# Kernel optimization log

Hardware: AMD Instinct MI355X
Metric: run time of the kernel (lower is better)

The kernel has to match this reference:

```python
import jax, jax.numpy as jnp
import numpy as np

B, N, E = 2, 2048, 1024
H = 16
D = E // H  # head_dim = 64
MLP = 4096
EPS = 1e-5


def _layernorm(x, g, b):
    mu = jnp.mean(x, axis=-1, keepdims=True)
    var = jnp.var(x, axis=-1, keepdims=True)
    return (x - mu) * jax.lax.rsqrt(var + EPS) * g + b


def setup_inputs() -> dict:
    key = jax.random.key(0)
    ks = jax.random.split(key, 12)
    s_e = 1.0 / np.sqrt(E)
    s_m = 1.0 / np.sqrt(MLP)
    return {
        "x": jax.random.normal(ks[0], (B, N, E), jnp.float32),
        "w_qkv": jax.random.uniform(ks[1], (E, 3 * E), jnp.float32, -s_e, s_e),
        "b_qkv": jax.random.uniform(ks[2], (3 * E,), jnp.float32, -s_e, s_e),
        "w_proj": jax.random.uniform(ks[3], (E, E), jnp.float32, -s_e, s_e),
        "b_proj": jax.random.uniform(ks[4], (E,), jnp.float32, -s_e, s_e),
        "g1": jnp.ones((E,), jnp.float32),
        "beta1": jnp.zeros((E,), jnp.float32),
        "g2": jnp.ones((E,), jnp.float32),
        "beta2": jnp.zeros((E,), jnp.float32),
        "w_fc1": jax.random.uniform(ks[5], (E, MLP), jnp.float32, -s_e, s_e),
        "b_fc1": jax.random.uniform(ks[6], (MLP,), jnp.float32, -s_e, s_e),
        "w_fc2": jax.random.uniform(ks[7], (MLP, E), jnp.float32, -s_m, s_m),
        "b_fc2": jax.random.uniform(ks[8], (E,), jnp.float32, -s_m, s_m),
    }


def reference(x, w_qkv, b_qkv, w_proj, b_proj, g1, beta1, g2, beta2,
              w_fc1, b_fc1, w_fc2, b_fc2):
    scale = D ** (-0.5)
    # --- attention block (pre-norm) ---
    h = _layernorm(x, g1, beta1)
    qkv = (h @ w_qkv + b_qkv).reshape(B, N, 3, H, D)
    q, k, v = (qkv[:, :, i].transpose(0, 2, 1, 3) for i in range(3))  # [B,H,N,D]
    scores = jnp.einsum("bhnd,bhmd->bhnm", q, k) * scale  # [B,H,N,N]
    attn = jax.nn.softmax(scores, axis=-1)
    out = jnp.einsum("bhnm,bhmd->bhnd", attn, v)
    out = out.transpose(0, 2, 1, 3).reshape(B, N, E)
    x = x + (out @ w_proj + b_proj)
    # --- MLP block (pre-norm, exact GELU as in torch default) ---
    h = _layernorm(x, g2, beta2)
    h = jax.nn.gelu(h @ w_fc1 + b_fc1, approximate=False) @ w_fc2 + b_fc2
    return x + h
```

## Files before the change

kernel.cpp:

```cpp
#include <hip/hip_runtime.h>
#include <hip/hip_bf16.h>
#include <cmath>


typedef __hip_bfloat16 bf16;
typedef __bf16 bf16x8 __attribute__((ext_vector_type(8)));
typedef __bf16 bf16x4v __attribute__((ext_vector_type(4)));
typedef float  f32x4  __attribute__((ext_vector_type(4)));

#define CB 2
#define CN 2048
#define CE 1024
#define CH 16
#define CD 64
#define CMLP 4096
#define CM (CB*CN)

#define PS 136

#define QPRE 0.18033688011112042f
#if __has_builtin(__builtin_amdgcn_exp2f)
#define EXP2(s) __builtin_amdgcn_exp2f(s)
#else
#define EXP2(s) __expf((s)*0.69314718055994531f)
#endif

__device__ __forceinline__ float b2f(bf16 v){ return __bfloat162float(v); }
__device__ __forceinline__ bf16  f2b(float v){ return __float2bfloat16(v); }

__device__ __forceinline__ void gl_lds16(const void* g, void* l){
  __builtin_amdgcn_global_load_lds((__attribute__((address_space(1))) void*)g,
                                   (__attribute__((address_space(3))) void*)l,
                                   16, 0, 0);
}

#define FENCE asm volatile("" ::: "memory")
#define BAR   do{ FENCE; __builtin_amdgcn_s_barrier(); FENCE; }while(0)
#define VMW6  asm volatile("s_waitcnt vmcnt(6)" ::: "memory")
#define VMW0  asm volatile("s_waitcnt vmcnt(0)" ::: "memory")

__global__ __launch_bounds__(256) void transpose4_k(
  const float* __restrict__ i0, bf16* __restrict__ o0,
  const float* __restrict__ i1, bf16* __restrict__ o1,
  const float* __restrict__ i2, bf16* __restrict__ o2,
  const float* __restrict__ i3, bf16* __restrict__ o3)
{
  __shared__ float tile[32][33];
  int t = blockIdx.x;
  const float* in; bf16* out; int K, N, nx;
  if(t < 3072){            in=i0; out=o0; K=1024; N=3072; nx=96; }
  else if(t < 4096){ t-=3072; in=i1; out=o1; K=1024; N=1024; nx=32; }
  else if(t < 8192){ t-=4096; in=i2; out=o2; K=1024; N=4096; nx=128; }
  else {             t-=8192; in=i3; out=o3; K=4096; N=1024; nx=32; }
  const int n0 = (t%nx)*32, k0 = (t/nx)*32;
  const int tx = threadIdx.x & 31;
  const int ty = threadIdx.x >> 5;
  #pragma unroll
  for(int i=0;i<32;i+=8) tile[ty+i][tx] = in[(size_t)(k0+ty+i)*N + n0+tx];
  __syncthreads();
  #pragma unroll
  for(int i=0;i<32;i+=8) out[(size_t)(n0+ty+i)*K + k0+tx] = f2b(tile[tx][ty+i]);
}

__global__ __launch_bounds__(256) void ln_k(const float* __restrict__ x,
                                            const float* __restrict__ g,
                                            const float* __restrict__ be,
                                            bf16* __restrict__ out){
  const int row = blockIdx.x;
  const int t = threadIdx.x;
  const float4 v4 = ((const float4*)(x + (size_t)row*CE))[t];
  float v[4] = {v4.x, v4.y, v4.z, v4.w};
  float s=0.f, s2=0.f;
  #pragma unroll
  for(int i=0;i<4;i++){ s+=v[i]; s2+=v[i]*v[i]; }
  #pragma unroll
  for(int off=32; off>0; off>>=1){ s += __shfl_down(s,off); s2 += __shfl_down(s2,off); }
  __shared__ float red[8];
  __shared__ float mu_s, rs_s;
  const int wv=t>>6, ln=t&63;
  if(ln==0){ red[wv]=s; red[4+wv]=s2; }
  __syncthreads();
  if(t==0){
    float S=red[0]+red[1]+red[2]+red[3], S2=red[4]+red[5]+red[6]+red[7];
    float mu=S/CE;
    mu_s=mu; rs_s=rsqrtf(S2/CE - mu*mu + 1e-5f);
  }
  __syncthreads();
  const float mu=mu_s, rs=rs_s;
  #pragma unroll
  for(int i=0;i<4;i++){
    int c=t*4+i;
    out[(size_t)row*CE+c] = f2b((v[i]-mu)*rs*g[c] + be[c]);
  }
}

#define EP_QKV 0
#define EP_RES 1
#define EP_GELU 2

template<int MODE, int BN>
__global__ __launch_bounds__(256,2) void gemm_k(
  const bf16* __restrict__ A, const bf16* __restrict__ BT,
  const float* __restrict__ bias, const float* __restrict__ res,
  float* __restrict__ Cf, bf16* __restrict__ Cb,
  bf16* __restrict__ Cq, bf16* __restrict__ Ck, bf16* __restrict__ Cv,
  int Ksz, int Nsz)
{
  constexpr int NJ = BN/32;
  constexpr int NBUF = (BN==64) ? 3 : 2;
  __shared__ __align__(16) bf16 Alds[NBUF][128*64];
  __shared__ __align__(16) bf16 Blds[NBUF][BN*64];
  const int tid = threadIdx.x;
  const int wave = tid>>6, lane = tid&63;
  const int m16 = lane&15, quad = lane>>4;
  const int wi = wave>>1, wj = wave&1;

  const int lin = blockIdx.x + gridDim.x*blockIdx.y;
  const int m_idx = (lin&7) + 8*((lin>>3)&3);
  const int n_idx = lin>>5;
  const size_t m0 = (size_t)m_idx*128;
  const size_t n0 = (size_t)n_idx*BN;

  f32x4 acc[4][NJ] = {};

  const int srow8 = lane>>3;
  const int schk  = ((lane&7)^srow8)*8;
  const bf16* pA = A  + (m0 + 32*wave      + srow8)*(size_t)Ksz + schk;
  const bf16* pB = BT + (n0 + (BN/4)*wave  + srow8)*(size_t)Ksz + schk;

  auto stage = [&](int buf, const bf16* gA, const bf16* gB){
    bf16* lA = &Alds[buf][wave*2048];
    bf16* lB = &Blds[buf][wave*(BN*16)];
    #pragma unroll
    for(int j=0;j<4;j++)  gl_lds16(gA + (size_t)(j*8)*Ksz, lA + j*512);
    #pragma unroll
    for(int j=0;j<NJ;j++) gl_lds16(gB + (size_t)(j*8)*Ksz, lB + j*512);
  };
  auto compute = [&](int buf){
    #pragma unroll
    for(int w=0;w<2;w++){
      const int sw = (m16&7);
      bf16x8 af[4], bfr[NJ];
      #pragma unroll
      for(int i=0;i<4;i++){
        const int row = wi*64+16*i+m16;
        af[i] = *(const bf16x8*)(&Alds[buf][row*64 + ((w*4+quad)^sw)*8]);
      }
      #pragma unroll
      for(int j=0;j<NJ;j++){
        const int row = wj*(BN/2)+16*j+m16;
        bfr[j] = *(const bf16x8*)(&Blds[buf][row*64 + ((w*4+quad)^sw)*8]);
      }
      #pragma unroll
      for(int i=0;i<4;i++)
        #pragma unroll
        for(int j=0;j<NJ;j++)
          acc[i][j] = __builtin_amdgcn_mfma_f32_16x16x32_bf16(af[i], bfr[j], acc[i][j], 0,0,0);
    }
  };

  const int kIters = Ksz/64;
  if constexpr (BN==64){
    stage(0, pA, pB); pA += 64; pB += 64;
    stage(1, pA, pB); pA += 64; pB += 64;
    int bc = 0, bs = 2;
    for(int kb=0; kb<kIters; ++kb){
      if(kb==kIters-1){ VMW0; } else { VMW6; }
      BAR;
      if(kb+2<kIters){ stage(bs, pA, pB); pA += 64; pB += 64; }
      compute(bc);
      bc = (bc==2)?0:bc+1;
      bs = (bs==2)?0:bs+1;
    }
  } else {
    stage(0, pA, pB); pA += 64; pB += 64;
    for(int kb=0; kb<kIters; ++kb){
      __syncthreads();
      if(kb+1<kIters){ stage((kb+1)&1, pA, pB); pA += 64; pB += 64; }
      compute(kb&1);
    }
  }

  #pragma unroll
  for(int i=0;i<4;i++){
    #pragma unroll
    for(int j=0;j<NJ;j++){
      const int col = (int)n0 + wj*(BN/2) + 16*j + m16;
      const float bcol = bias[col];
      #pragma unroll
      for(int r=0;r<4;r++){
        const int row = (int)m0 + wi*64 + 16*i + quad*4 + r;
        float v = acc[i][j][r] + bcol;
        if constexpr (MODE==EP_QKV){
          const int b = row>>11, n = row&2047;
          const int which = col>>10, cc = col&1023;
          const int h = cc>>6, d = cc&63;
          if(which==0)      Cq[(((size_t)(b*CH+h))*CN+n)*CD + d] = f2b(v*QPRE);
          else if(which==1) Ck[(((size_t)(b*CH+h))*CN+n)*CD + d] = f2b(v);
          else              Cv[(((size_t)(b*CH+h))*CD+d)*CN + n] = f2b(v);
        } else if constexpr (MODE==EP_RES){
          v += res[(size_t)row*Nsz+col];
          Cf[(size_t)row*Nsz+col] = v;
        } else {
          const float u2 = 1.5957691216f*(v + 0.044715f*v*v*v);
          v = v * (1.f/(1.f + __expf(-u2)));
          Cb[(size_t)row*Nsz+col] = f2b(v);
        }
      }
    }
  }
}

__global__ __launch_bounds__(256,2) void attn_k(
  const bf16* __restrict__ Q, const bf16* __restrict__ Kx,
  const bf16* __restrict__ Vt, bf16* __restrict__ O)
{
  const int lin = blockIdx.x + gridDim.x*blockIdx.y;
  const int bh = (lin&7) + 8*(lin>>7);
  const int qblk = (lin>>3)&15;
  const int b = bh>>4, h = bh&15;
  const int tid = threadIdx.x;
  const int wave = tid>>6, lane = tid&63;
  const int m16 = lane&15, quad = lane>>4;
  const int sw = m16&7;
  const int q0 = qblk*128 + wave*32;

  const bf16* Qb = Q  + (size_t)bh*CN*CD;
  const bf16* Kb = Kx + (size_t)bh*CN*CD;
  const bf16* Vb = Vt + (size_t)bh*CD*CN;

  bf16x8 qf[2][2];
  #pragma unroll
  for(int g=0;g<2;g++){
    const bf16* qp = Qb + (size_t)(q0+g*16+m16)*CD + quad*8;
    qf[g][0] = *(const bf16x8*)(qp);
    qf[g][1] = *(const bf16x8*)(qp + 32);
  }

  bf16x8 onesv;
  #pragma unroll
  for(int i=0;i<8;i++) onesv[i] = (__bf16)1.0f;

  f32x4 lacc[2] = {};
  f32x4 oacc[2][4] = {};

  __shared__ __align__(16) bf16 Klds[128*64];
  __shared__ __align__(16) bf16 Vlds[64*128];
  __shared__ __align__(16) bf16 Plds[4][32*PS];
  bf16* Pw = &Plds[wave][0];

  const int krow = wave*32 + (lane>>3);
  const int kchk = (lane&7) ^ (lane>>3);
  const bf16* pK = Kb + (size_t)krow*CD + kchk*8;
  const int vrow = wave*16 + (lane>>4);
  const bf16* pV[4];
  #pragma unroll
  for(int j=0;j<4;j++){
    const int ck = (lane&15) ^ ((j*4 + (lane>>4)) & 7);
    pV[j] = Vb + (size_t)(vrow + j*4)*CN + ck*8;
  }
  bf16* lK = Klds + wave*2048;
  bf16* lV = Vlds + wave*2048;

  for(int kt=0; kt<CN; kt+=128){
    __syncthreads();
    #pragma unroll
    for(int j=0;j<4;j++){
      gl_lds16(pK + (size_t)j*8*CD, lK + j*512);
      gl_lds16(pV[j],               lV + j*512);
      pV[j] += 128;
    }
    pK += (size_t)128*CD;
    __syncthreads();

    f32x4 sf0[8], sf1[8];
    #pragma unroll
    for(int f=0;f<8;f++){
      const bf16* kb = Klds + (f*16+m16)*64;
      bf16x8 k0 = *(const bf16x8*)(kb + ((quad   ^ sw)*8));
      bf16x8 k1 = *(const bf16x8*)(kb + (((quad+4)^ sw)*8));
      f32x4 t0 = {}, t1 = {};
      t0 = __builtin_amdgcn_mfma_f32_16x16x32_bf16(k0, qf[0][0], t0, 0,0,0);
      t0 = __builtin_amdgcn_mfma_f32_16x16x32_bf16(k1, qf[0][1], t0, 0,0,0);
      t1 = __builtin_amdgcn_mfma_f32_16x16x32_bf16(k0, qf[1][0], t1, 0,0,0);
      t1 = __builtin_amdgcn_mfma_f32_16x16x32_bf16(k1, qf[1][1], t1, 0,0,0);
      sf0[f]=t0; sf1[f]=t1;
    }
    #pragma unroll
    for(int f=0;f<8;f++){
      bf16x4v p0, p1;
      #pragma unroll
      for(int r=0;r<4;r++){
        p0[r] = (__bf16)EXP2(sf0[f][r]);
        p1[r] = (__bf16)EXP2(sf1[f][r]);
      }
      *(bf16x4v*)(Pw + (size_t)m16*PS       + f*16 + quad*4) = p0;
      *(bf16x4v*)(Pw + (size_t)(16+m16)*PS  + f*16 + quad*4) = p1;
    }
    asm volatile("s_waitcnt lgkmcnt(0)" ::: "memory");
    #pragma unroll
    for(int c=0;c<4;c++){
      const bf16x8 ap0 = *(const bf16x8*)(Pw + (size_t)m16*PS      + c*32 + quad*8);
      const bf16x8 ap1 = *(const bf16x8*)(Pw + (size_t)(16+m16)*PS + c*32 + quad*8);
      lacc[0] = __builtin_amdgcn_mfma_f32_16x16x32_bf16(ap0, onesv, lacc[0], 0,0,0);
      lacc[1] = __builtin_amdgcn_mfma_f32_16x16x32_bf16(ap1, onesv, lacc[1], 0,0,0);
      #pragma unroll
      for(int dt=0;dt<4;dt++){
        const int d = dt*16+m16;
        bf16x8 bv = *(const bf16x8*)(Vlds + d*128 + (((c*4+quad) ^ sw)*8));
        oacc[0][dt] = __builtin_amdgcn_mfma_f32_16x16x32_bf16(ap0, bv, oacc[0][dt], 0,0,0);
        oacc[1][dt] = __builtin_amdgcn_mfma_f32_16x16x32_bf16(ap1, bv, oacc[1][dt], 0,0,0);
      }
    }
  }
  #pragma unroll
  for(int g=0;g<2;g++){
    float linv[4];
    #pragma unroll
    for(int r=0;r<4;r++) linv[r] = 1.f / lacc[g][r];
    #pragma unroll
    for(int dt=0;dt<4;dt++){
      #pragma unroll
      for(int r=0;r<4;r++){
        const int row = q0 + g*16 + quad*4 + r;
        O[((size_t)(b*CN+row))*CE + h*CD + dt*16 + m16] = f2b(oacc[g][dt][r]*linv[r]);
      }
    }
  }
}

extern "C" void kernel_launch(void* const* d_in, const int* in_sizes, int n_in,
                              void* d_out, int out_size, void* d_ws, size_t ws_size,
                              hipStream_t stream)
{
  (void)in_sizes; (void)n_in; (void)out_size; (void)ws_size;
  const float* x     = (const float*)d_in[0];
  const float* w_qkv = (const float*)d_in[1];
  const float* b_qkv = (const float*)d_in[2];
  const float* w_proj= (const float*)d_in[3];
  const float* b_proj= (const float*)d_in[4];
  const float* g1    = (const float*)d_in[5];
  const float* be1   = (const float*)d_in[6];
  const float* g2    = (const float*)d_in[7];
  const float* be2   = (const float*)d_in[8];
  const float* w_fc1 = (const float*)d_in[9];
  const float* b_fc1 = (const float*)d_in[10];
  const float* w_fc2 = (const float*)d_in[11];
  const float* b_fc2 = (const float*)d_in[12];
  float* out = (float*)d_out;

  char* ws = (char*)d_ws;
  size_t off = 0;
  auto alloc = [&](size_t bytes)->char*{
    char* p = ws + off;
    off += (bytes + 255) & ~(size_t)255;
    return p;
  };
  bf16* wqkvT = (bf16*)alloc((size_t)3072*1024*2);
  bf16* wprojT= (bf16*)alloc((size_t)1024*1024*2);
  bf16* wfc1T = (bf16*)alloc((size_t)4096*1024*2);
  bf16* wfc2T = (bf16*)alloc((size_t)1024*4096*2);
  bf16* h1    = (bf16*)alloc((size_t)CM*CE*2);
  bf16* q     = (bf16*)alloc((size_t)CM*CE*2);
  bf16* kk    = (bf16*)alloc((size_t)CM*CE*2);
  bf16* vT    = (bf16*)alloc((size_t)CM*CE*2);
  bf16* aO    = (bf16*)alloc((size_t)CM*CE*2);
  float* x2   = (float*)alloc((size_t)CM*CE*4);
  bf16* hmlp  = q;

  transpose4_k<<<12288,256,0,stream>>>(w_qkv, wqkvT, w_proj, wprojT,
                                       w_fc1, wfc1T, w_fc2, wfc2T);

  ln_k<<<CM,256,0,stream>>>(x, g1, be1, h1);
  gemm_k<EP_QKV,128><<<dim3(3072/128, CM/128),256,0,stream>>>(
      h1, wqkvT, b_qkv, nullptr, nullptr, nullptr, q, kk, vT, 1024, 3072);
  attn_k<<<dim3(CN/128, CB*CH),256,0,stream>>>(q, kk, vT, aO);
  gemm_k<EP_RES,64><<<dim3(1024/64, CM/128),256,0,stream>>>(
      aO, wprojT, b_proj, x, x2, nullptr, nullptr,nullptr,nullptr, 1024, 1024);
  ln_k<<<CM,256,0,stream>>>(x2, g2, be2, h1);
  gemm_k<EP_GELU,128><<<dim3(4096/128, CM/128),256,0,stream>>>(
      h1, wfc1T, b_fc1, nullptr, nullptr, hmlp, nullptr,nullptr,nullptr, 1024, 4096);
  gemm_k<EP_RES,64><<<dim3(1024/64, CM/128),256,0,stream>>>(
      hmlp, wfc2T, b_fc2, x2, out, nullptr, nullptr,nullptr,nullptr, 4096, 1024);
}
```

Before: 336.5 us.

## Add 128x128 triple-buffered GEMM kernel for projection and FC2 residual GEMMs

Adds a new GEMM kernel with 128x128 output tiles and a 64-wide K step, staged through three LDS buffers via direct global-to-LDS loads so two stages stay in flight. It replaces the 128x64-tile gemm_k for the attention-output projection and the FC2 residual GEMMs. The goal is more data reuse per block and deeper load/compute overlap. The cost is that the N=1024 GEMMs launch half as many blocks (256), which may leave compute units underused, and the large LDS footprint allows only one block per CU.

```diff
diff --git a/kernel.cpp b/kernel.cpp
--- a/kernel.cpp
+++ b/kernel.cpp
@@ -36,6 +36,7 @@
 
 #define FENCE asm volatile("" ::: "memory")
 #define BAR   do{ FENCE; __builtin_amdgcn_s_barrier(); FENCE; }while(0)
+#define VMW8  asm volatile("s_waitcnt vmcnt(8)" ::: "memory")
 #define VMW6  asm volatile("s_waitcnt vmcnt(6)" ::: "memory")
 #define VMW0  asm volatile("s_waitcnt vmcnt(0)" ::: "memory")
 
@@ -206,6 +207,87 @@
           v = v * (1.f/(1.f + __expf(-u2)));
           Cb[(size_t)row*Nsz+col] = f2b(v);
         }
+      }
+    }
+  }
+}
+
+__global__ __launch_bounds__(256,1) void gemmbig_k(
+  const bf16* __restrict__ A, const bf16* __restrict__ BT,
+  const float* __restrict__ bias, const float* __restrict__ res,
+  float* __restrict__ Cf, int Ksz, int Nsz)
+{
+  __shared__ __align__(16) bf16 Alds[3][128*64];
+  __shared__ __align__(16) bf16 Blds[3][128*64];
+  const int tid = threadIdx.x;
+  const int wave = tid>>6, lane = tid&63;
+  const int m16 = lane&15, quad = lane>>4;
+  const int sw = m16&7;
+  const int wi = wave>>1, wj = wave&1;
+
+  const int lin = blockIdx.x + gridDim.x*blockIdx.y;
+  const int m_idx = (lin&7) + 8*((lin>>3)&3);
+  const int n_idx = lin>>5;
+  const size_t m0 = (size_t)m_idx*128;
+  const size_t n0 = (size_t)n_idx*128;
+
+  f32x4 acc[4][4] = {};
+
+  const int srow8 = lane>>3;
+  const int schk  = ((lane&7)^srow8)*8;
+  const bf16* pA = A  + (m0 + 32*wave + srow8)*(size_t)Ksz + schk;
+  const bf16* pB = BT + (n0 + 32*wave + srow8)*(size_t)Ksz + schk;
+
+  auto stage = [&](int buf){
+    bf16* lA = &Alds[buf][wave*2048];
+    bf16* lB = &Blds[buf][wave*2048];
+    #pragma unroll
+    for(int j=0;j<4;j++){
+      gl_lds16(pA + (size_t)(j*8)*Ksz, lA + j*512);
+      gl_lds16(pB + (size_t)(j*8)*Ksz, lB + j*512);
+    }
+    pA += 64; pB += 64;
+  };
+  auto compute = [&](int buf){
+    #pragma unroll
+    for(int w=0;w<2;w++){
+      bf16x8 af[4], bfr[4];
+      #pragma unroll
+      for(int i=0;i<4;i++)
+        af[i] = *(const bf16x8*)(&Alds[buf][(wi*64+16*i+m16)*64 + ((w*4+quad)^sw)*8]);
+      #pragma unroll
+      for(int j=0;j<4;j++)
+        bfr[j] = *(const bf16x8*)(&Blds[buf][(wj*64+16*j+m16)*64 + ((w*4+quad)^sw)*8]);
+      #pragma unroll
+      for(int i=0;i<4;i++)
+        #pragma unroll
+        for(int j=0;j<4;j++)
+          acc[i][j] = __builtin_amdgcn_mfma_f32_16x16x32_bf16(af[i], bfr[j], acc[i][j], 0,0,0);
+    }
+  };
+
+  const int kIters = Ksz/64;
+  stage(0); stage(1);
+  int bc = 0, bs = 2;
+  for(int kb=0; kb<kIters; ++kb){
+    if(kb==kIters-1){ VMW0; } else { VMW8; }
+    BAR;
+    if(kb+2<kIters){ stage(bs); }
+    compute(bc);
+    bc = (bc==2)?0:bc+1;
+    bs = (bs==2)?0:bs+1;
+  }
+
+  #pragma unroll
+  for(int i=0;i<4;i++){
+    #pragma unroll
+    for(int j=0;j<4;j++){
+      const int col = (int)n0 + wj*64 + 16*j + m16;
+      const float bcol = bias[col];
+      #pragma unroll
+      for(int r=0;r<4;r++){
+        const int row = (int)m0 + wi*64 + 16*i + quad*4 + r;
+        Cf[(size_t)row*Nsz+col] = acc[i][j][r] + bcol + res[(size_t)row*Nsz+col];
       }
     }
   }
@@ -375,11 +457,11 @@
   gemm_k<EP_QKV,128><<<dim3(3072/128, CM/128),256,0,stream>>>(
       h1, wqkvT, b_qkv, nullptr, nullptr, nullptr, q, kk, vT, 1024, 3072);
   attn_k<<<dim3(CN/128, CB*CH),256,0,stream>>>(q, kk, vT, aO);
-  gemm_k<EP_RES,64><<<dim3(1024/64, CM/128),256,0,stream>>>(
-      aO, wprojT, b_proj, x, x2, nullptr, nullptr,nullptr,nullptr, 1024, 1024);
+  gemmbig_k<<<dim3(1024/128, CM/128),256,0,stream>>>(
+      aO, wprojT, b_proj, x, x2, 1024, 1024);
   ln_k<<<CM,256,0,stream>>>(x2, g2, be2, h1);
   gemm_k<EP_GELU,128><<<dim3(4096/128, CM/128),256,0,stream>>>(
       h1, wfc1T, b_fc1, nullptr, nullptr, hmlp, nullptr,nullptr,nullptr, 1024, 4096);
-  gemm_k<EP_RES,64><<<dim3(1024/64, CM/128),256,0,stream>>>(
-      hmlp, wfc2T, b_fc2, x2, out, nullptr, nullptr,nullptr,nullptr, 4096, 1024);
-}
+  gemmbig_k<<<dim3(1024/128, CM/128),256,0,stream>>>(
+      hmlp, wfc2T, b_fc2, x2, out, 4096, 1024);
+}
```

New measurement: 350.8 us. 1.04x slower.

## Double-buffer attention K/V tiles and fuse first layernorm into weight prep

Applied to the files above, without the earlier changes.

The attention kernel now uses 64-key tiles with two LDS buffers and prefetches the next K/V tile while computing on the current one. This drops one of the two barriers per iteration and overlaps global loads with MFMA work. Separately, the first layernorm is folded into the weight transpose launch as extra blocks, which removes one kernel launch. The smaller tiles double the number of loop iterations and barriers, and the double buffering relies on a single barrier being enough to protect buffer reuse.

```diff
diff --git a/kernel.cpp b/kernel.cpp
--- a/kernel.cpp
+++ b/kernel.cpp
@@ -16,7 +16,7 @@
 #define CMLP 4096
 #define CM (CB*CN)
 
-#define PS 136
+#define PS2 72
 
 #define QPRE 0.18033688011112042f
 #if __has_builtin(__builtin_amdgcn_exp2f)
@@ -39,22 +39,53 @@
 #define VMW6  asm volatile("s_waitcnt vmcnt(6)" ::: "memory")
 #define VMW0  asm volatile("s_waitcnt vmcnt(0)" ::: "memory")
 
-__global__ __launch_bounds__(256) void transpose4_k(
+__global__ __launch_bounds__(256) void prep_k(
   const float* __restrict__ i0, bf16* __restrict__ o0,
   const float* __restrict__ i1, bf16* __restrict__ o1,
   const float* __restrict__ i2, bf16* __restrict__ o2,
-  const float* __restrict__ i3, bf16* __restrict__ o3)
+  const float* __restrict__ i3, bf16* __restrict__ o3,
+  const float* __restrict__ x,  const float* __restrict__ g,
+  const float* __restrict__ be, bf16* __restrict__ lnout)
 {
   __shared__ float tile[32][33];
+  __shared__ float red[8];
+  __shared__ float mu_s, rs_s;
   int t = blockIdx.x;
+  const int tid = threadIdx.x;
+  if(t >= 12288){
+    const int row = t - 12288;
+    const float4 v4 = ((const float4*)(x + (size_t)row*CE))[tid];
+    float v[4] = {v4.x, v4.y, v4.z, v4.w};
+    float s=0.f, s2=0.f;
+    #pragma unroll
+    for(int i=0;i<4;i++){ s+=v[i]; s2+=v[i]*v[i]; }
+    #pragma unroll
+    for(int off=32; off>0; off>>=1){ s += __shfl_down(s,off); s2 += __shfl_down(s2,off); }
+    const int wv=tid>>6, ln=tid&63;
+    if(ln==0){ red[wv]=s; red[4+wv]=s2; }
+    __syncthreads();
+    if(tid==0){
+      float S=red[0]+red[1]+red[2]+red[3], S2=red[4]+red[5]+red[6]+red[7];
+      float mu=S/CE;
+      mu_s=mu; rs_s=rsqrtf(S2/CE - mu*mu + 1e-5f);
+    }
+    __syncthreads();
+    const float mu=mu_s, rs=rs_s;
+    #pragma unroll
+    for(int i=0;i<4;i++){
+      int c=tid*4+i;
+      lnout[(size_t)row*CE+c] = f2b((v[i]-mu)*rs*g[c] + be[c]);
+    }
+    return;
+  }
   const float* in; bf16* out; int K, N, nx;
   if(t < 3072){            in=i0; out=o0; K=1024; N=3072; nx=96; }
   else if(t < 4096){ t-=3072; in=i1; out=o1; K=1024; N=1024; nx=32; }
   else if(t < 8192){ t-=4096; in=i2; out=o2; K=1024; N=4096; nx=128; }
   else {             t-=8192; in=i3; out=o3; K=4096; N=1024; nx=32; }
   const int n0 = (t%nx)*32, k0 = (t/nx)*32;
-  const int tx = threadIdx.x & 31;
-  const int ty = threadIdx.x >> 5;
+  const int tx = tid & 31;
+  const int ty = tid >> 5;
   #pragma unroll
   for(int i=0;i<32;i+=8) tile[ty+i][tx] = in[(size_t)(k0+ty+i)*N + n0+tx];
   __syncthreads();
@@ -244,39 +275,37 @@
   f32x4 lacc[2] = {};
   f32x4 oacc[2][4] = {};
 
-  __shared__ __align__(16) bf16 Klds[128*64];
-  __shared__ __align__(16) bf16 Vlds[64*128];
-  __shared__ __align__(16) bf16 Plds[4][32*PS];
+  __shared__ __align__(16) bf16 Klds[2][64*64];
+  __shared__ __align__(16) bf16 Vlds[2][64*64];
+  __shared__ __align__(16) bf16 Plds[4][32*PS2];
   bf16* Pw = &Plds[wave][0];
 
-  const int krow = wave*32 + (lane>>3);
-  const int kchk = (lane&7) ^ (lane>>3);
-  const bf16* pK = Kb + (size_t)krow*CD + kchk*8;
-  const int vrow = wave*16 + (lane>>4);
-  const bf16* pV[4];
-  #pragma unroll
-  for(int j=0;j<4;j++){
-    const int ck = (lane&15) ^ ((j*4 + (lane>>4)) & 7);
-    pV[j] = Vb + (size_t)(vrow + j*4)*CN + ck*8;
-  }
-  bf16* lK = Klds + wave*2048;
-  bf16* lV = Vlds + wave*2048;
-
-  for(int kt=0; kt<CN; kt+=128){
+  const int srow8 = lane>>3;
+  const int kchk  = (lane&7) ^ srow8;
+  const bf16* pK = Kb + (size_t)(wave*16 + srow8)*CD + kchk*8;
+  const bf16* pV = Vb + (size_t)(wave*16 + srow8)*CN + kchk*8;
+  const int ldso = wave*1024;
+
+  auto stage = [&](int buf, int kt){
+    #pragma unroll
+    for(int j=0;j<2;j++){
+      gl_lds16(pK + ((size_t)kt + (size_t)j*8)*CD, &Klds[buf][ldso + j*512]);
+      gl_lds16(pV + (size_t)j*8*CN + kt,           &Vlds[buf][ldso + j*512]);
+    }
+  };
+
+  stage(0, 0);
+  const int nT = CN/64;
+  for(int t=0; t<nT; ++t){
     __syncthreads();
-    #pragma unroll
-    for(int j=0;j<4;j++){
-      gl_lds16(pK + (size_t)j*8*CD, lK + j*512);
-      gl_lds16(pV[j],               lV + j*512);
-      pV[j] += 128;
-    }
-    pK += (size_t)128*CD;
-    __syncthreads();
-
-    f32x4 sf0[8], sf1[8];
-    #pragma unroll
-    for(int f=0;f<8;f++){
-      const bf16* kb = Klds + (f*16+m16)*64;
+    if(t+1<nT) stage((t+1)&1, (t+1)*64);
+    const bf16* Kl = &Klds[t&1][0];
+    const bf16* Vl = &Vlds[t&1][0];
+
+    f32x4 sf0[4], sf1[4];
+    #pragma unroll
+    for(int f=0;f<4;f++){
+      const bf16* kb = Kl + (f*16+m16)*64;
       bf16x8 k0 = *(const bf16x8*)(kb + ((quad   ^ sw)*8));
       bf16x8 k1 = *(const bf16x8*)(kb + (((quad+4)^ sw)*8));
       f32x4 t0 = {}, t1 = {};
@@ -287,27 +316,27 @@
       sf0[f]=t0; sf1[f]=t1;
     }
     #pragma unroll
-    for(int f=0;f<8;f++){
+    for(int f=0;f<4;f++){
       bf16x4v p0, p1;
       #pragma unroll
       for(int r=0;r<4;r++){
         p0[r] = (__bf16)EXP2(sf0[f][r]);
         p1[r] = (__bf16)EXP2(sf1[f][r]);
       }
-      *(bf16x4v*)(Pw + (size_t)m16*PS       + f*16 + quad*4) = p0;
-      *(bf16x4v*)(Pw + (size_t)(16+m16)*PS  + f*16 + quad*4) = p1;
+      *(bf16x4v*)(Pw + (size_t)m16*PS2      + f*16 + quad*4) = p0;
+      *(bf16x4v*)(Pw + (size_t)(16+m16)*PS2 + f*16 + quad*4) = p1;
     }
     asm volatile("s_waitcnt lgkmcnt(0)" ::: "memory");
     #pragma unroll
-    for(int c=0;c<4;c++){
-      const bf16x8 ap0 = *(const bf16x8*)(Pw + (size_t)m16*PS      + c*32 + quad*8);
-      const bf16x8 ap1 = *(const bf16x8*)(Pw + (size_t)(16+m16)*PS + c*32 + quad*8);
+    for(int c=0;c<2;c++){
+      const bf16x8 ap0 = *(const bf16x8*)(Pw + (size_t)m16*PS2      + c*32 + quad*8);
+      const bf16x8 ap1 = *(const bf16x8*)(Pw + (size_t)(16+m16)*PS2 + c*32 + quad*8);
       lacc[0] = __builtin_amdgcn_mfma_f32_16x16x32_bf16(ap0, onesv, lacc[0], 0,0,0);
       lacc[1] = __builtin_amdgcn_mfma_f32_16x16x32_bf16(ap1, onesv, lacc[1], 0,0,0);
       #pragma unroll
       for(int dt=0;dt<4;dt++){
         const int d = dt*16+m16;
-        bf16x8 bv = *(const bf16x8*)(Vlds + d*128 + (((c*4+quad) ^ sw)*8));
+        bf16x8 bv = *(const bf16x8*)(Vl + d*64 + (((c*4+quad) ^ sw)*8));
         oacc[0][dt] = __builtin_amdgcn_mfma_f32_16x16x32_bf16(ap0, bv, oacc[0][dt], 0,0,0);
         oacc[1][dt] = __builtin_amdgcn_mfma_f32_16x16x32_bf16(ap1, bv, oacc[1][dt], 0,0,0);
       }
@@ -368,10 +397,10 @@
   float* x2   = (float*)alloc((size_t)CM*CE*4);
   bf16* hmlp  = q;
 
-  transpose4_k<<<12288,256,0,stream>>>(w_qkv, wqkvT, w_proj, wprojT,
-                                       w_fc1, wfc1T, w_fc2, wfc2T);
-
-  ln_k<<<CM,256,0,stream>>>(x, g1, be1, h1);
+  prep_k<<<12288+CM,256,0,stream>>>(w_qkv, wqkvT, w_proj, wprojT,
+                                    w_fc1, wfc1T, w_fc2, wfc2T,
+                                    x, g1, be1, h1);
+
   gemm_k<EP_QKV,128><<<dim3(3072/128, CM/128),256,0,stream>>>(
       h1, wqkvT, b_qkv, nullptr, nullptr, nullptr, q, kk, vT, 1024, 3072);
   attn_k<<<dim3(CN/128, CB*CH),256,0,stream>>>(q, kk, vT, aO);
```

New measurement: 333.8 us (median of 2 runs). About the same (-0.8%).
